# Kernel tuning notes

Measured on AMD Instinct MI355X. Metric: run time of the kernel, lower is better.

The kernel has to match this reference:

```python
import jax, jax.numpy as jnp
import numpy as np

N_NODES = 50000
NEG_SLOPE = 0.2

def _segment_softmax(e, seg, n):
    m = jax.ops.segment_max(e, seg, num_segments=n)
    ex = jnp.exp(e - m[seg])
    s = jax.ops.segment_sum(ex, seg, num_segments=n)
    return ex / s[seg]

def _gatv2_layer(x, src, dst, n, Wl, bl, Wr, br, att):
    # GATv2 (heads=1): e_ij = att . leaky_relu(Wl x_j + Wr x_i); msg = alpha * Wl x_j
    xl = x @ Wl + bl            # [N, D] source transform
    xr = x @ Wr + br            # [N, D] target transform
    h = jax.nn.leaky_relu(xl[src] + xr[dst], NEG_SLOPE)  # [E, D]
    e = h @ att                 # [E]
    alpha = _segment_softmax(e, dst, n)
    out = jax.ops.segment_sum(alpha[:, None] * xl[src], dst, num_segments=n)
    return out

def setup_inputs() -> dict:
    key = jax.random.key(0)
    ks = jax.random.split(key, 16)
    N, E, Q, F, D, H = N_NODES, 800000, 200000, 128, 250, 256
    def glorot(k, shape):
        fan = shape[0] + shape[-1]
        return jax.random.uniform(k, shape, jnp.float32, -1.0, 1.0) * np.sqrt(6.0 / fan)
    return {
        "x": jax.random.normal(ks[0], (N, F), jnp.float32),
        "edge_index": jax.random.randint(ks[1], (2, E), 0, N, jnp.int32),
        "query": jax.random.randint(ks[2], (Q, 2), 0, N, jnp.int32),
        "W1l": glorot(ks[3], (F, D)), "b1l": jnp.zeros((D,), jnp.float32),
        "W1r": glorot(ks[4], (F, D)), "b1r": jnp.zeros((D,), jnp.float32),
        "att1": glorot(ks[5], (D,)),
        "W2l": glorot(ks[6], (D, D)), "b2l": jnp.zeros((D,), jnp.float32),
        "W2r": glorot(ks[7], (D, D)), "b2r": jnp.zeros((D,), jnp.float32),
        "att2": glorot(ks[8], (D,)),
        "Wm1": glorot(ks[9], (2 * D, H)), "bm1": jnp.zeros((H,), jnp.float32),
        "Wm2": glorot(ks[10], (H, 1)), "bm2": jnp.zeros((1,), jnp.float32),
    }

def reference(x, edge_index, query, W1l, b1l, W1r, b1r, att1,
              W2l, b2l, W2r, b2r, att2, Wm1, bm1, Wm2, bm2):
    n = x.shape[0]
    # add self loops (PyG default add_self_loops=True)
    loops = jnp.arange(n, dtype=edge_index.dtype)
    src = jnp.concatenate([edge_index[0], loops])
    dst = jnp.concatenate([edge_index[1], loops])
    h = _gatv2_layer(x, src, dst, n, W1l, b1l, W1r, b1r, att1)
    h = jax.nn.relu(h)
    emb = _gatv2_layer(h, src, dst, n, W2l, b2l, W2r, b2r, att2)
    # edge-prediction head: gather pair embeddings, concat, MLP
    pair = jnp.concatenate([emb[query[:, 0]], emb[query[:, 1]]], axis=1)  # [Q, 2D]
    out = jax.nn.relu(pair @ Wm1 + bm1)
    out = jax.nn.relu(out @ Wm2 + bm2)
    return out
```

## Files before the change

### kernel.cpp

```cpp
#include <hip/hip_runtime.h>
#include <hip/hip_fp16.h>
#include <math.h>
#include <stdint.h>

#define NN 50000
#define NE 800000
#define ET (NE + NN)
#define FIN 128
#define DD 250
#define HD 256
#define NQ 200000
#define NEG_SLOPE 0.2f
#define NPW 4

typedef unsigned short u16;
typedef __attribute__((ext_vector_type(4))) float f32x4;
typedef _Float16 h2v __attribute__((ext_vector_type(2)));
typedef _Float16 f16x8 __attribute__((ext_vector_type(8)));

union H2U { h2v h; unsigned int u; };

__device__ __forceinline__ u16 f2h(float v) {
    __half h = __float2half(v);
    return *reinterpret_cast<u16*>(&h);
}
__device__ __forceinline__ float4 ld4h(const u16* p) {
    uint2 r = *(const uint2*)p;
    __half2 a = *(__half2*)&r.x;
    __half2 b = *(__half2*)&r.y;
    float2 fa = __half22float2(a), fb = __half22float2(b);
    return make_float4(fa.x, fa.y, fb.x, fb.y);
}
__device__ __forceinline__ h2v hmax2v(h2v a, h2v b) {
    return __builtin_elementwise_max(a, b);
}


#define DPPMOV(v, ctrl, rm) \
    ((unsigned int)__builtin_amdgcn_update_dpp(0, (int)(v), (ctrl), (rm), 0xF, true))

__device__ __forceinline__ unsigned int h2_wave_sum63(h2v x) {
    H2U u, t; u.h = x;
    t.u = DPPMOV(u.u, 0x111, 0xF); u.h = u.h + t.h;
    t.u = DPPMOV(u.u, 0x112, 0xF); u.h = u.h + t.h;
    t.u = DPPMOV(u.u, 0x114, 0xF); u.h = u.h + t.h;
    t.u = DPPMOV(u.u, 0x118, 0xF); u.h = u.h + t.h;
    t.u = DPPMOV(u.u, 0x142, 0xA); u.h = u.h + t.h;
    t.u = DPPMOV(u.u, 0x143, 0xC); u.h = u.h + t.h;
    return (unsigned int)__builtin_amdgcn_readlane((int)u.u, 63);
}

__device__ __forceinline__ float f32_wave_sum63(float x) {
    union FU { float f; unsigned int u; } a, t, o;
    a.f = x;
    t.u = DPPMOV(a.u, 0x111, 0xF); a.f += t.f;
    t.u = DPPMOV(a.u, 0x112, 0xF); a.f += t.f;
    t.u = DPPMOV(a.u, 0x114, 0xF); a.f += t.f;
    t.u = DPPMOV(a.u, 0x118, 0xF); a.f += t.f;
    t.u = DPPMOV(a.u, 0x142, 0xA); a.f += t.f;
    t.u = DPPMOV(a.u, 0x143, 0xC); a.f += t.f;
    o.u = (unsigned int)__builtin_amdgcn_readlane((int)a.u, 63);
    return o.f;
}


__global__ __launch_bounds__(256) void scan1_kernel(
    int* __restrict__ cnt, int* __restrict__ rowptr, int* __restrict__ bsum)
{
    __shared__ int buf[256];
    int t = threadIdx.x;
    int i = blockIdx.x * 256 + t;
    int v = (i < NN) ? cnt[i] : 0;
    if (i < NN) cnt[i] = 0;
    buf[t] = v;
    __syncthreads();
#pragma unroll
    for (int off = 1; off < 256; off <<= 1) {
        int add = (t >= off) ? buf[t - off] : 0;
        __syncthreads();
        buf[t] += add;
        __syncthreads();
    }
    if (i < NN) rowptr[i] = buf[t] - v;
    if (t == 255) bsum[blockIdx.x] = buf[255];
}

__global__ __launch_bounds__(256) void scan2_kernel(
    int* __restrict__ bsum, int* __restrict__ rowptr, int nb)
{
    __shared__ int buf[256];
    int t = threadIdx.x;
    int v = (t < nb) ? bsum[t] : 0;
    buf[t] = v;
    __syncthreads();
#pragma unroll
    for (int off = 1; off < 256; off <<= 1) {
        int add = (t >= off) ? buf[t - off] : 0;
        __syncthreads();
        buf[t] += add;
        __syncthreads();
    }
    if (t < nb) bsum[t] = buf[t] - v;
    if (t == 255) rowptr[NN] = buf[255];
}

__global__ __launch_bounds__(256) void scan3_kernel(
    int* __restrict__ rowptr, const int* __restrict__ bsum)
{
    int i = blockIdx.x * 256 + threadIdx.x;
    if (i < NN) rowptr[i] += bsum[blockIdx.x];
}

__global__ void scatter_kernel(const int* __restrict__ ei,
                               const int* __restrict__ rowptr,
                               int* __restrict__ fill,
                               int* __restrict__ ssrc) {
    int k = blockIdx.x * 256 + threadIdx.x;
    if (k >= ET) return;
    int s, d;
    if (k < NE) { s = ei[k]; d = ei[NE + k]; }
    else        { s = k - NE; d = k - NE; }
    int pos = rowptr[d] + atomicAdd(&fill[d], 1);
    ssrc[pos] = s << 9;
}


#define CONVX_BLOCKS 3125
#define CNT_BLOCKS ((ET + 255) / 256)

__global__ __launch_bounds__(256) void conv_all(
    const float* __restrict__ x, const int* __restrict__ ei,
    u16* __restrict__ Asp,
    const float* __restrict__ W1l, const float* __restrict__ W1r,
    const float* __restrict__ W2l, const float* __restrict__ W2r,
    const float* __restrict__ Wm1,
    const float* __restrict__ att1, const float* __restrict__ att2,
    u16* __restrict__ W1lT, u16* __restrict__ W1rT,
    u16* __restrict__ W2lT, u16* __restrict__ W2rT,
    u16* __restrict__ WmtT, u16* __restrict__ WmbT,
    u16* __restrict__ atth1, u16* __restrict__ atth2,
    int* __restrict__ cnt)
{
    if (blockIdx.x < CONVX_BLOCKS) {
        int tid = blockIdx.x * 256 + threadIdx.x;
        size_t idx = (size_t)tid * 8;
        if (idx >= (size_t)NN * FIN) return;
        float4 v0 = *(const float4*)(x + idx);
        float4 v1 = *(const float4*)(x + idx + 4);
        ushort4 o0, o1;
        o0.x = f2h(v0.x); o0.y = f2h(v0.y); o0.z = f2h(v0.z); o0.w = f2h(v0.w);
        o1.x = f2h(v1.x); o1.y = f2h(v1.y); o1.z = f2h(v1.z); o1.w = f2h(v1.w);
        *(ushort4*)(Asp + idx) = o0;
        *(ushort4*)(Asp + idx + 4) = o1;
        return;
    }
    int b = blockIdx.x - CONVX_BLOCKS;
    if (b < 1280) {
        const float* W; int K, N, koff, kshift, b0; u16* ot;
        if (b < 128)       { W = W1l; K = FIN; N = DD; koff = 0;  kshift = 7; b0 = 0;    ot = W1lT; }
        else if (b < 256)  { W = W1r; K = FIN; N = DD; koff = 0;  kshift = 7; b0 = 128;  ot = W1rT; }
        else if (b < 512)  { W = W2l; K = DD;  N = DD; koff = 0;  kshift = 8; b0 = 256;  ot = W2lT; }
        else if (b < 768)  { W = W2r; K = DD;  N = DD; koff = 0;  kshift = 8; b0 = 512;  ot = W2rT; }
        else if (b < 1024) { W = Wm1; K = DD;  N = HD; koff = 0;  kshift = 8; b0 = 768;  ot = WmtT; }
        else               { W = Wm1; K = DD;  N = HD; koff = DD; kshift = 8; b0 = 1024; ot = WmbT; }
        int id = (b - b0) * 256 + threadIdx.x;
        int Kp = 1 << kshift;
        int n = id >> kshift, k = id & (Kp - 1);
        float v = (n < N && k < K) ? W[(size_t)(k + koff) * N + n] : 0.f;
        ot[id] = f2h(v);
        return;
    }
    if (b < 1282) {
        const float* a = (b == 1280) ? att1 : att2;
        u16* o = (b == 1280) ? atth1 : atth2;
        int id = threadIdx.x;
        o[id] = f2h(id < DD ? a[id] : 0.f);
        return;
    }
    int k = (b - 1282) * 256 + threadIdx.x;
    if (k >= ET) return;
    int d = (k < NE) ? ei[NE + k] : (k - NE);
    atomicAdd(&cnt[d], 1);
}


#define AP 40

__global__ __launch_bounds__(512) void gemm_pair(
    const u16* __restrict__ A, int Kp,
    const u16* __restrict__ B0, const u16* __restrict__ B1,
    const float* __restrict__ bias0, const float* __restrict__ bias1,
    void* __restrict__ C0v, void* __restrict__ C1v, int M, int N, int fmt)
{
    __shared__ u16 AS[128][AP], B0S[256][AP], B1S[256][AP];

    int row0 = blockIdx.x * 128;
    int t = threadIdx.x;
    int lane = t & 63, w = t >> 6;
    int wr = w >> 2, wc = w & 3;
    int quad = lane >> 4, rr = lane & 15;

    f32x4 acc0[4][4], acc1[4][4];
#pragma unroll
    for (int i = 0; i < 4; i++)
#pragma unroll
        for (int j = 0; j < 4; j++) {
            acc0[i][j] = (f32x4){0.f, 0.f, 0.f, 0.f};
            acc1[i][j] = (f32x4){0.f, 0.f, 0.f, 0.f};
        }

    int arow = t >> 2, akc = (t & 3) * 8;
    bool aok = (row0 + arow) < M;
    const u16* pA   = A  + (size_t)(row0 + arow) * Kp + akc;
    int brow = t >> 2, bkc = akc;
    const u16* pB0a = B0 + (size_t)brow * Kp + bkc;
    const u16* pB0b = pB0a + (size_t)128 * Kp;
    const u16* pB1a = B1 + (size_t)brow * Kp + bkc;
    const u16* pB1b = pB1a + (size_t)128 * Kp;

    for (int k0 = 0; k0 < Kp; k0 += 32) {
        f16x8 a{};
        if (aok) a = *(const f16x8*)(pA + k0);
        *(f16x8*)&AS[arow][akc]            = a;
        *(f16x8*)&B0S[brow][bkc]           = *(const f16x8*)(pB0a + k0);
        *(f16x8*)&B0S[brow + 128][bkc]     = *(const f16x8*)(pB0b + k0);
        *(f16x8*)&B1S[brow][bkc]           = *(const f16x8*)(pB1a + k0);
        *(f16x8*)&B1S[brow + 128][bkc]     = *(const f16x8*)(pB1b + k0);
        __syncthreads();

        f16x8 fA[4];
#pragma unroll
        for (int fi = 0; fi < 4; fi++) {
            int r = wr * 64 + fi * 16 + rr;
            fA[fi] = *(const f16x8*)&AS[r][quad * 8];
        }
#pragma unroll
        for (int fj = 0; fj < 4; fj++) {
            int c = wc * 64 + fj * 16 + rr;
            f16x8 b0 = *(const f16x8*)&B0S[c][quad * 8];
            f16x8 b1 = *(const f16x8*)&B1S[c][quad * 8];
#pragma unroll
            for (int fi = 0; fi < 4; fi++) {
                acc0[fi][fj] = __builtin_amdgcn_mfma_f32_16x16x32_f16(fA[fi], b0, acc0[fi][fj], 0, 0, 0);
                acc1[fi][fj] = __builtin_amdgcn_mfma_f32_16x16x32_f16(fA[fi], b1, acc1[fi][fj], 0, 0, 0);
            }
        }
        __syncthreads();
    }

#pragma unroll
    for (int fj = 0; fj < 4; fj++) {
        int gc = wc * 64 + fj * 16 + rr;
        if (gc >= N) continue;
        float bb0 = bias0 ? bias0[gc] : 0.f;
        float bb1 = bias1 ? bias1[gc] : 0.f;
#pragma unroll
        for (int fi = 0; fi < 4; fi++) {
#pragma unroll
            for (int r = 0; r < 4; r++) {
                int grr = row0 + wr * 64 + fi * 16 + quad * 4 + r;
                if (grr < M) {
                    float v0 = acc0[fi][fj][r] + bb0;
                    float v1 = acc1[fi][fj][r] + bb1;
                    if (fmt & 1) ((u16*)C0v)[(size_t)grr * 256 + gc] = f2h(v0);
                    else         ((float*)C0v)[(size_t)grr * N + gc] = v0;
                    if (fmt & 2) ((u16*)C1v)[(size_t)grr * 256 + gc] = f2h(v1);
                    else         ((float*)C1v)[(size_t)grr * N + gc] = v1;
                }
            }
        }
    }
}


__global__ __launch_bounds__(256) void fused_edge_kernel(
    const int* __restrict__ rowptr, const int* __restrict__ ssrc,
    const u16* __restrict__ xl16, const u16* __restrict__ xr16,
    const u16* __restrict__ atth,
    u16* __restrict__ Oh, int dorelu)
{
    int wid = blockIdx.x * 4 + (threadIdx.x >> 6);
    int base = wid * NPW;
    if (base >= NN) return;
    int lane = threadIdx.x & 63;
    int d0 = lane * 4;
    int lb = d0 * 2;

    uint2 atr = *(const uint2*)&atth[d0];
    h2v at0h = *(h2v*)&atr.x, at1h = *(h2v*)&atr.y;
    const h2v c02 = {(_Float16)0.2f, (_Float16)0.2f};
    const char* xlb = (const char*)xl16;

    auto ldrow = [&](int o) -> uint2 {
        return *(const uint2*)(xlb + o + lb);
    };

    uint2 xrr = *(const uint2*)&xr16[(size_t)base * 256 + d0];

    for (int k = 0; k < NPW; k++) {
        int i = base + k;
        if (i >= NN) break;
        h2v xr0h = *(h2v*)&xrr.x, xr1h = *(h2v*)&xrr.y;
        int beg = __builtin_amdgcn_readfirstlane(rowptr[i]);
        int end = __builtin_amdgcn_readfirstlane(rowptr[i + 1]);

        float m = -1e30f, ssum = 0.f;
        float4 acc = make_float4(0.f, 0.f, 0.f, 0.f);

        auto edge_score = [&](uint2 g) -> float {
            h2v x0 = *(h2v*)&g.x, x1 = *(h2v*)&g.y;
            h2v s = x0 + xr0h; s = hmax2v(s, s * c02);
            float e = __builtin_amdgcn_fdot2(s, at0h, 0.f, false);
            s = x1 + xr1h; s = hmax2v(s, s * c02);
            return __builtin_amdgcn_fdot2(s, at1h, e, false);
        };
        auto single_update = [&](uint2 g) {
            float e = f32_wave_sum63(edge_score(g));
            h2v x0 = *(h2v*)&g.x, x1 = *(h2v*)&g.y;
            float nm = fmaxf(m, e);
            float sc = __expf(m - nm);
            float w = __expf(e - nm);
            acc.x = fmaf(w, (float)x0.x, acc.x * sc);
            acc.y = fmaf(w, (float)x0.y, acc.y * sc);
            acc.z = fmaf(w, (float)x1.x, acc.z * sc);
            acc.w = fmaf(w, (float)x1.y, acc.w * sc);
            ssum = fmaf(ssum, sc, w);
            m = nm;
        };

        int p = beg;
        if (p + 3 < end) {
            int o0 = __builtin_amdgcn_readfirstlane(ssrc[p]);
            int o1 = __builtin_amdgcn_readfirstlane(ssrc[p + 1]);
            int o2 = __builtin_amdgcn_readfirstlane(ssrc[p + 2]);
            int o3 = __builtin_amdgcn_readfirstlane(ssrc[p + 3]);
            uint2 c0 = ldrow(o0), c1 = ldrow(o1), c2 = ldrow(o2), c3 = ldrow(o3);
            bool hn = (p + 7 < end);
            int no0 = 0, no1 = 0, no2 = 0, no3 = 0;
            if (hn) {
                no0 = __builtin_amdgcn_readfirstlane(ssrc[p + 4]);
                no1 = __builtin_amdgcn_readfirstlane(ssrc[p + 5]);
                no2 = __builtin_amdgcn_readfirstlane(ssrc[p + 6]);
                no3 = __builtin_amdgcn_readfirstlane(ssrc[p + 7]);
            }
            for (;;) {
                uint2 n0, n1, n2, n3;
                if (hn) {
                    n0 = ldrow(no0); n1 = ldrow(no1); n2 = ldrow(no2); n3 = ldrow(no3);
                }
                bool hnn = (p + 11 < end);
                int nn0 = 0, nn1 = 0, nn2 = 0, nn3 = 0;
                if (hnn) {
                    nn0 = __builtin_amdgcn_readfirstlane(ssrc[p + 8]);
                    nn1 = __builtin_amdgcn_readfirstlane(ssrc[p + 9]);
                    nn2 = __builtin_amdgcn_readfirstlane(ssrc[p + 10]);
                    nn3 = __builtin_amdgcn_readfirstlane(ssrc[p + 11]);
                }

                h2v x00 = *(h2v*)&c0.x, x01 = *(h2v*)&c0.y;
                h2v x10 = *(h2v*)&c1.x, x11 = *(h2v*)&c1.y;
                h2v x20 = *(h2v*)&c2.x, x21 = *(h2v*)&c2.y;
                h2v x30 = *(h2v*)&c3.x, x31 = *(h2v*)&c3.y;

                h2v s;
                float e0, e1, e2, e3;
                s = x00 + xr0h; s = hmax2v(s, s * c02);
                e0 = __builtin_amdgcn_fdot2(s, at0h, 0.f, false);
                s = x01 + xr1h; s = hmax2v(s, s * c02);
                e0 = __builtin_amdgcn_fdot2(s, at1h, e0, false);
                s = x10 + xr0h; s = hmax2v(s, s * c02);
                e1 = __builtin_amdgcn_fdot2(s, at0h, 0.f, false);
                s = x11 + xr1h; s = hmax2v(s, s * c02);
                e1 = __builtin_amdgcn_fdot2(s, at1h, e1, false);
                s = x20 + xr0h; s = hmax2v(s, s * c02);
                e2 = __builtin_amdgcn_fdot2(s, at0h, 0.f, false);
                s = x21 + xr1h; s = hmax2v(s, s * c02);
                e2 = __builtin_amdgcn_fdot2(s, at1h, e2, false);
                s = x30 + xr0h; s = hmax2v(s, s * c02);
                e3 = __builtin_amdgcn_fdot2(s, at0h, 0.f, false);
                s = x31 + xr1h; s = hmax2v(s, s * c02);
                e3 = __builtin_amdgcn_fdot2(s, at1h, e3, false);

                H2U u01, u23, r01, r23;
                u01.h.x = (_Float16)e0; u01.h.y = (_Float16)e1;
                u23.h.x = (_Float16)e2; u23.h.y = (_Float16)e3;
                r01.u = h2_wave_sum63(u01.h);
                r23.u = h2_wave_sum63(u23.h);
                float es0 = (float)r01.h.x, es1 = (float)r01.h.y;
                float es2 = (float)r23.h.x, es3 = (float)r23.h.y;

                float nm = fmaxf(fmaxf(m, es0), fmaxf(fmaxf(es1, es2), es3));
                float sc = __expf(m - nm);
                float w0 = __expf(es0 - nm);
                float w1 = __expf(es1 - nm);
                float w2 = __expf(es2 - nm);
                float w3 = __expf(es3 - nm);
                float ax0 = fmaf(w1, (float)x10.x, w0 * (float)x00.x);
                float ax1 = fmaf(w3, (float)x30.x, w2 * (float)x20.x);
                float ay0 = fmaf(w1, (float)x10.y, w0 * (float)x00.y);
                float ay1 = fmaf(w3, (float)x30.y, w2 * (float)x20.y);
                float az0 = fmaf(w1, (float)x11.x, w0 * (float)x01.x);
                float az1 = fmaf(w3, (float)x31.x, w2 * (float)x21.x);
                float aw0 = fmaf(w1, (float)x11.y, w0 * (float)x01.y);
                float aw1 = fmaf(w3, (float)x31.y, w2 * (float)x21.y);
                acc.x = fmaf(acc.x, sc, ax0 + ax1);
                acc.y = fmaf(acc.y, sc, ay0 + ay1);
                acc.z = fmaf(acc.z, sc, az0 + az1);
                acc.w = fmaf(acc.w, sc, aw0 + aw1);
                ssum = fmaf(ssum, sc, (w0 + w1) + (w2 + w3));
                m = nm;

                p += 4;
                if (!hn) break;
                c0 = n0; c1 = n1; c2 = n2; c3 = n3;
                no0 = nn0; no1 = nn1; no2 = nn2; no3 = nn3;
                hn = hnn;
            }
        }

        if (k + 1 < NPW && i + 1 < NN)
            xrr = *(const uint2*)&xr16[(size_t)(i + 1) * 256 + d0];

        int rem = end - p;
        if (rem > 0) {
            int o0 = __builtin_amdgcn_readfirstlane(ssrc[p]);
            int o1 = 0, o2 = 0;
            if (rem > 1) o1 = __builtin_amdgcn_readfirstlane(ssrc[p + 1]);
            if (rem > 2) o2 = __builtin_amdgcn_readfirstlane(ssrc[p + 2]);
            uint2 g0 = ldrow(o0);
            uint2 g1, g2;
            if (rem > 1) g1 = ldrow(o1);
            if (rem > 2) g2 = ldrow(o2);
            single_update(g0);
            if (rem > 1) single_update(g1);
            if (rem > 2) single_update(g2);
        }

        float inv = 1.f / ssum;
        acc.x *= inv; acc.y *= inv; acc.z *= inv; acc.w *= inv;
        if (dorelu) {
            acc.x = fmaxf(acc.x, 0.f); acc.y = fmaxf(acc.y, 0.f);
            acc.z = fmaxf(acc.z, 0.f); acc.w = fmaxf(acc.w, 0.f);
        }
        size_t obase = (size_t)i * 256 + d0;
        ushort4 hv;
        hv.x = f2h(acc.x); hv.y = f2h(acc.y); hv.z = f2h(acc.z); hv.w = f2h(acc.w);
        *(ushort4*)&Oh[obase] = hv;
    }
}


__global__ __launch_bounds__(256) void query_kernel(
    const int* __restrict__ qry, const u16* __restrict__ Ptop,
    const u16* __restrict__ Pbot, const float* __restrict__ Wm2,
    const float* __restrict__ bm2, float* __restrict__ out)
{
    int q = (blockIdx.x * 4 + (threadIdx.x >> 6)) * 2;
    if (q >= NQ) return;
    int lane = threadIdx.x & 63;
    int a0 = __builtin_amdgcn_readfirstlane(qry[q * 2 + 0]);
    int b0 = __builtin_amdgcn_readfirstlane(qry[q * 2 + 1]);
    int a1 = __builtin_amdgcn_readfirstlane(qry[q * 2 + 2]);
    int b1 = __builtin_amdgcn_readfirstlane(qry[q * 2 + 3]);
    float4 w  = *(const float4*)&Wm2[lane * 4];
    float4 t0 = ld4h(&Ptop[(size_t)a0 * HD + lane * 4]);
    float4 v0 = ld4h(&Pbot[(size_t)b0 * HD + lane * 4]);
    float4 t1 = ld4h(&Ptop[(size_t)a1 * HD + lane * 4]);
    float4 v1 = ld4h(&Pbot[(size_t)b1 * HD + lane * 4]);
    float s0 = fmaxf(t0.x + v0.x, 0.f) * w.x + fmaxf(t0.y + v0.y, 0.f) * w.y
             + fmaxf(t0.z + v0.z, 0.f) * w.z + fmaxf(t0.w + v0.w, 0.f) * w.w;
    float s1 = fmaxf(t1.x + v1.x, 0.f) * w.x + fmaxf(t1.y + v1.y, 0.f) * w.y
             + fmaxf(t1.z + v1.z, 0.f) * w.z + fmaxf(t1.w + v1.w, 0.f) * w.w;
    s0 = f32_wave_sum63(s0);
    s1 = f32_wave_sum63(s1);
    if (lane == 0) {
        float bb = bm2[0];
        out[q] = fmaxf(s0 + bb, 0.f);
        if (q + 1 < NQ) out[q + 1] = fmaxf(s1 + bb, 0.f);
    }
}


extern "C" void kernel_launch(void* const* d_in, const int* in_sizes, int n_in,
                              void* d_out, int out_size, void* d_ws, size_t ws_size,
                              hipStream_t stream) {
    const float* x    = (const float*)d_in[0];
    const int*   ei   = (const int*)d_in[1];
    const int*   qry  = (const int*)d_in[2];
    const float* W1l  = (const float*)d_in[3];
    const float* b1l  = (const float*)d_in[4];
    const float* W1r  = (const float*)d_in[5];
    const float* b1r  = (const float*)d_in[6];
    const float* att1 = (const float*)d_in[7];
    const float* W2l  = (const float*)d_in[8];
    const float* b2l  = (const float*)d_in[9];
    const float* W2r  = (const float*)d_in[10];
    const float* b2r  = (const float*)d_in[11];
    const float* att2 = (const float*)d_in[12];
    const float* Wm1  = (const float*)d_in[13];
    const float* bm1  = (const float*)d_in[14];
    const float* Wm2  = (const float*)d_in[15];
    const float* bm2  = (const float*)d_in[16];
    float* out = (float*)d_out;

    u16* xl16    = (u16*)d_ws;
    u16* xr16    = xl16 + (size_t)NN * 256;
    int* rowptr  = (int*)(xr16 + (size_t)NN * 256);
    int* fill    = rowptr + NN + 1;
    int* ssrc    = fill + NN;
    int* bsum    = ssrc + ET;
    u16* atth1   = (u16*)(bsum + 256);
    u16* atth2   = atth1 + 256;
    uintptr_t wp = (uintptr_t)(atth2 + 256);
    wp = (wp + 63) & ~(uintptr_t)63;
    u16* W1lT = (u16*)wp;
    u16* W1rT = W1lT + 256 * 128;
    u16* W2lT = W1rT + 256 * 128;
    u16* W2rT = W2lT + 65536;
    u16* WmtT = W2rT + 65536;
    u16* WmbT = WmtT + 65536;
    u16* Asp  = WmbT + 65536;
    u16* Ptop16 = xl16;
    u16* Pbot16 = xr16;

    dim3 blk(256);
    int gET = (ET + 255) / 256;
    int gNode = (NN + 4 * NPW - 1) / (4 * NPW);
    int nb = (NN + 255) / 256;
    int gg = (NN + 127) / 128;

    hipMemsetAsync(fill, 0, (size_t)NN * sizeof(int), stream);
    conv_all<<<CONVX_BLOCKS + 1282 + gET, blk, 0, stream>>>(x, ei, Asp,
        W1l, W1r, W2l, W2r, Wm1, att1, att2,
        W1lT, W1rT, W2lT, W2rT, WmtT, WmbT, atth1, atth2, fill);

    scan1_kernel<<<nb, blk, 0, stream>>>(fill, rowptr, bsum);
    scan2_kernel<<<1, blk, 0, stream>>>(bsum, rowptr, nb);
    scan3_kernel<<<nb, blk, 0, stream>>>(rowptr, bsum);
    scatter_kernel<<<gET, blk, 0, stream>>>(ei, rowptr, fill, ssrc);

    gemm_pair<<<gg, dim3(512), 0, stream>>>(Asp, 128, W1lT, W1rT,
                                      b1l, b1r, (void*)xl16, (void*)xr16, NN, DD, 3);
    fused_edge_kernel<<<gNode, blk, 0, stream>>>(rowptr, ssrc, xl16, xr16, atth1, Asp, 1);

    gemm_pair<<<gg, dim3(512), 0, stream>>>(Asp, 256, W2lT, W2rT,
                                      b2l, b2r, (void*)xl16, (void*)xr16, NN, DD, 3);
    fused_edge_kernel<<<gNode, blk, 0, stream>>>(rowptr, ssrc, xl16, xr16, atth2, Asp, 0);

    gemm_pair<<<gg, dim3(512), 0, stream>>>(Asp, 256, WmtT, WmbT,
                                      bm1, (const float*)nullptr, (void*)Ptop16, (void*)Pbot16, NN, HD, 3);

    query_kernel<<<(NQ / 2 + 3) / 4, blk, 0, stream>>>(qry, Ptop16, Pbot16, Wm2, bm2, out);
}
```

Measured before the change: 530.6 us.

## Split each node's edges across two waves and merge, single-kernel scan

New measurement: 633.5 us. 19.4% more time.

```diff
diff --git a/kernel.cpp b/kernel.cpp
--- a/kernel.cpp
+++ b/kernel.cpp
@@ -11,7 +11,6 @@
 #define HD 256
 #define NQ 200000
 #define NEG_SLOPE 0.2f
-#define NPW 4
 
 typedef unsigned short u16;
 typedef __attribute__((ext_vector_type(4))) float f32x4;
@@ -64,51 +63,32 @@
 }
 
 
-__global__ __launch_bounds__(256) void scan1_kernel(
-    int* __restrict__ cnt, int* __restrict__ rowptr, int* __restrict__ bsum)
+__global__ __launch_bounds__(1024) void scan_all(
+    int* __restrict__ cnt, int* __restrict__ rowptr)
 {
-    __shared__ int buf[256];
+    __shared__ int buf[1024];
     int t = threadIdx.x;
-    int i = blockIdx.x * 256 + t;
-    int v = (i < NN) ? cnt[i] : 0;
-    if (i < NN) cnt[i] = 0;
-    buf[t] = v;
+    const int CH = (NN + 1023) / 1024;
+    int lo = t * CH, hi = lo + CH;
+    if (hi > NN) hi = NN;
+    int s = 0;
+    for (int j = lo; j < hi; j++) s += cnt[j];
+    buf[t] = s;
     __syncthreads();
-#pragma unroll
-    for (int off = 1; off < 256; off <<= 1) {
+    for (int off = 1; off < 1024; off <<= 1) {
         int add = (t >= off) ? buf[t - off] : 0;
         __syncthreads();
         buf[t] += add;
         __syncthreads();
     }
-    if (i < NN) rowptr[i] = buf[t] - v;
-    if (t == 255) bsum[blockIdx.x] = buf[255];
-}
-
-__global__ __launch_bounds__(256) void scan2_kernel(
-    int* __restrict__ bsum, int* __restrict__ rowptr, int nb)
-{
-    __shared__ int buf[256];
-    int t = threadIdx.x;
-    int v = (t < nb) ? bsum[t] : 0;
-    buf[t] = v;
-    __syncthreads();
-#pragma unroll
-    for (int off = 1; off < 256; off <<= 1) {
-        int add = (t >= off) ? buf[t - off] : 0;
-        __syncthreads();
-        buf[t] += add;
-        __syncthreads();
-    }
-    if (t < nb) bsum[t] = buf[t] - v;
-    if (t == 255) rowptr[NN] = buf[255];
-}
-
-__global__ __launch_bounds__(256) void scan3_kernel(
-    int* __restrict__ rowptr, const int* __restrict__ bsum)
-{
-    int i = blockIdx.x * 256 + threadIdx.x;
-    if (i < NN) rowptr[i] += bsum[blockIdx.x];
+    int run = buf[t] - s;
+    for (int j = lo; j < hi; j++) {
+        int c = cnt[j];
+        rowptr[j] = run;
+        run += c;
+        cnt[j] = 0;
+    }
+    if (t == 1023) rowptr[NN] = buf[1023];
 }
 
 __global__ void scatter_kernel(const int* __restrict__ ei,
@@ -279,10 +259,14 @@
     const u16* __restrict__ atth,
     u16* __restrict__ Oh, int dorelu)
 {
-    int wid = blockIdx.x * 4 + (threadIdx.x >> 6);
-    int base = wid * NPW;
-    if (base >= NN) return;
-    int lane = threadIdx.x & 63;
+    __shared__ float accS[2][2][4][64];
+    __shared__ float msS[2][2][2];
+
+    int t = threadIdx.x;
+    int np = t >> 7;
+    int h  = (t >> 6) & 1;
+    int lane = t & 63;
+    int i = blockIdx.x * 2 + np;
     int d0 = lane * 4;
     int lb = d0 * 2;
 
@@ -291,152 +275,170 @@
     const h2v c02 = {(_Float16)0.2f, (_Float16)0.2f};
     const char* xlb = (const char*)xl16;
 
+    uint2 xrr = *(const uint2*)&xr16[(size_t)i * 256 + d0];
+    h2v xr0h = *(h2v*)&xrr.x, xr1h = *(h2v*)&xrr.y;
+
+    int beg = __builtin_amdgcn_readfirstlane(rowptr[i]);
+    int end = __builtin_amdgcn_readfirstlane(rowptr[i + 1]);
+    int halfn = (end - beg + 1) >> 1;
+    int mb = beg + h * halfn;
+    int me = h ? end : (beg + halfn);
+
+    float m = -1e30f, ssum = 0.f;
+    float4 acc = make_float4(0.f, 0.f, 0.f, 0.f);
+
     auto ldrow = [&](int o) -> uint2 {
         return *(const uint2*)(xlb + o + lb);
     };
-
-    uint2 xrr = *(const uint2*)&xr16[(size_t)base * 256 + d0];
-
-    for (int k = 0; k < NPW; k++) {
-        int i = base + k;
-        if (i >= NN) break;
-        h2v xr0h = *(h2v*)&xrr.x, xr1h = *(h2v*)&xrr.y;
-        int beg = __builtin_amdgcn_readfirstlane(rowptr[i]);
-        int end = __builtin_amdgcn_readfirstlane(rowptr[i + 1]);
-
-        float m = -1e30f, ssum = 0.f;
-        float4 acc = make_float4(0.f, 0.f, 0.f, 0.f);
-
-        auto edge_score = [&](uint2 g) -> float {
-            h2v x0 = *(h2v*)&g.x, x1 = *(h2v*)&g.y;
-            h2v s = x0 + xr0h; s = hmax2v(s, s * c02);
-            float e = __builtin_amdgcn_fdot2(s, at0h, 0.f, false);
-            s = x1 + xr1h; s = hmax2v(s, s * c02);
-            return __builtin_amdgcn_fdot2(s, at1h, e, false);
-        };
-        auto single_update = [&](uint2 g) {
-            float e = f32_wave_sum63(edge_score(g));
-            h2v x0 = *(h2v*)&g.x, x1 = *(h2v*)&g.y;
-            float nm = fmaxf(m, e);
+    auto edge_score = [&](uint2 g) -> float {
+        h2v x0 = *(h2v*)&g.x, x1 = *(h2v*)&g.y;
+        h2v s = x0 + xr0h; s = hmax2v(s, s * c02);
+        float e = __builtin_amdgcn_fdot2(s, at0h, 0.f, false);
+        s = x1 + xr1h; s = hmax2v(s, s * c02);
+        return __builtin_amdgcn_fdot2(s, at1h, e, false);
+    };
+    auto single_update = [&](uint2 g) {
+        float e = f32_wave_sum63(edge_score(g));
+        h2v x0 = *(h2v*)&g.x, x1 = *(h2v*)&g.y;
+        float nm = fmaxf(m, e);
+        float sc = __expf(m - nm);
+        float w = __expf(e - nm);
+        acc.x = fmaf(w, (float)x0.x, acc.x * sc);
+        acc.y = fmaf(w, (float)x0.y, acc.y * sc);
+        acc.z = fmaf(w, (float)x1.x, acc.z * sc);
+        acc.w = fmaf(w, (float)x1.y, acc.w * sc);
+        ssum = fmaf(ssum, sc, w);
+        m = nm;
+    };
+
+    int p = mb;
+    if (p + 3 < me) {
+        int o0 = __builtin_amdgcn_readfirstlane(ssrc[p]);
+        int o1 = __builtin_amdgcn_readfirstlane(ssrc[p + 1]);
+        int o2 = __builtin_amdgcn_readfirstlane(ssrc[p + 2]);
+        int o3 = __builtin_amdgcn_readfirstlane(ssrc[p + 3]);
+        uint2 c0 = ldrow(o0), c1 = ldrow(o1), c2 = ldrow(o2), c3 = ldrow(o3);
+        bool hn = (p + 7 < me);
+        int no0 = 0, no1 = 0, no2 = 0, no3 = 0;
+        if (hn) {
+            no0 = __builtin_amdgcn_readfirstlane(ssrc[p + 4]);
+            no1 = __builtin_amdgcn_readfirstlane(ssrc[p + 5]);
+            no2 = __builtin_amdgcn_readfirstlane(ssrc[p + 6]);
+            no3 = __builtin_amdgcn_readfirstlane(ssrc[p + 7]);
+        }
+        for (;;) {
+            uint2 n0, n1, n2, n3;
+            if (hn) {
+                n0 = ldrow(no0); n1 = ldrow(no1); n2 = ldrow(no2); n3 = ldrow(no3);
+            }
+            bool hnn = (p + 11 < me);
+            int nn0 = 0, nn1 = 0, nn2 = 0, nn3 = 0;
+            if (hnn) {
+                nn0 = __builtin_amdgcn_readfirstlane(ssrc[p + 8]);
+                nn1 = __builtin_amdgcn_readfirstlane(ssrc[p + 9]);
+                nn2 = __builtin_amdgcn_readfirstlane(ssrc[p + 10]);
+                nn3 = __builtin_amdgcn_readfirstlane(ssrc[p + 11]);
+            }
+
+            h2v x00 = *(h2v*)&c0.x, x01 = *(h2v*)&c0.y;
+            h2v x10 = *(h2v*)&c1.x, x11 = *(h2v*)&c1.y;
+            h2v x20 = *(h2v*)&c2.x, x21 = *(h2v*)&c2.y;
+            h2v x30 = *(h2v*)&c3.x, x31 = *(h2v*)&c3.y;
+
+            h2v s;
+            float e0, e1, e2, e3;
+            s = x00 + xr0h; s = hmax2v(s, s * c02);
+            e0 = __builtin_amdgcn_fdot2(s, at0h, 0.f, false);
+            s = x01 + xr1h; s = hmax2v(s, s * c02);
+            e0 = __builtin_amdgcn_fdot2(s, at1h, e0, false);
+            s = x10 + xr0h; s = hmax2v(s, s * c02);
+            e1 = __builtin_amdgcn_fdot2(s, at0h, 0.f, false);
+            s = x11 + xr1h; s = hmax2v(s, s * c02);
+            e1 = __builtin_amdgcn_fdot2(s, at1h, e1, false);
+            s = x20 + xr0h; s = hmax2v(s, s * c02);
+            e2 = __builtin_amdgcn_fdot2(s, at0h, 0.f, false);
+            s = x21 + xr1h; s = hmax2v(s, s * c02);
+            e2 = __builtin_amdgcn_fdot2(s, at1h, e2, false);
+            s = x30 + xr0h; s = hmax2v(s, s * c02);
+            e3 = __builtin_amdgcn_fdot2(s, at0h, 0.f, false);
+            s = x31 + xr1h; s = hmax2v(s, s * c02);
+            e3 = __builtin_amdgcn_fdot2(s, at1h, e3, false);
+
+            H2U u01, u23, r01, r23;
+            u01.h.x = (_Float16)e0; u01.h.y = (_Float16)e1;
+            u23.h.x = (_Float16)e2; u23.h.y = (_Float16)e3;
+            r01.u = h2_wave_sum63(u01.h);
+            r23.u = h2_wave_sum63(u23.h);
+            float es0 = (float)r01.h.x, es1 = (float)r01.h.y;
+            float es2 = (float)r23.h.x, es3 = (float)r23.h.y;
+
+            float nm = fmaxf(fmaxf(m, es0), fmaxf(fmaxf(es1, es2), es3));
             float sc = __expf(m - nm);
-            float w = __expf(e - nm);
-            acc.x = fmaf(w, (float)x0.x, acc.x * sc);
-            acc.y = fmaf(w, (float)x0.y, acc.y * sc);
-            acc.z = fmaf(w, (float)x1.x, acc.z * sc);
-            acc.w = fmaf(w, (float)x1.y, acc.w * sc);
-            ssum = fmaf(ssum, sc, w);
+            float w0 = __expf(es0 - nm);
+            float w1 = __expf(es1 - nm);
+            float w2 = __expf(es2 - nm);
+            float w3 = __expf(es3 - nm);
+            float ax0 = fmaf(w1, (float)x10.x, w0 * (float)x00.x);
+            float ax1 = fmaf(w3, (float)x30.x, w2 * (float)x20.x);
+            float ay0 = fmaf(w1, (float)x10.y, w0 * (float)x00.y);
+            float ay1 = fmaf(w3, (float)x30.y, w2 * (float)x20.y);
+            float az0 = fmaf(w1, (float)x11.x, w0 * (float)x01.x);
+            float az1 = fmaf(w3, (float)x31.x, w2 * (float)x21.x);
+            float aw0 = fmaf(w1, (float)x11.y, w0 * (float)x01.y);
+            float aw1 = fmaf(w3, (float)x31.y, w2 * (float)x21.y);
+            acc.x = fmaf(acc.x, sc, ax0 + ax1);
+            acc.y = fmaf(acc.y, sc, ay0 + ay1);
+            acc.z = fmaf(acc.z, sc, az0 + az1);
+            acc.w = fmaf(acc.w, sc, aw0 + aw1);
+            ssum = fmaf(ssum, sc, (w0 + w1) + (w2 + w3));
             m = nm;
-        };
-
-        int p = beg;
-        if (p + 3 < end) {
-            int o0 = __builtin_amdgcn_readfirstlane(ssrc[p]);
-            int o1 = __builtin_amdgcn_readfirstlane(ssrc[p + 1]);
-            int o2 = __builtin_amdgcn_readfirstlane(ssrc[p + 2]);
-            int o3 = __builtin_amdgcn_readfirstlane(ssrc[p + 3]);
-            uint2 c0 = ldrow(o0), c1 = ldrow(o1), c2 = ldrow(o2), c3 = ldrow(o3);
-            bool hn = (p + 7 < end);
-            int no0 = 0, no1 = 0, no2 = 0, no3 = 0;
-            if (hn) {
-                no0 = __builtin_amdgcn_readfirstlane(ssrc[p + 4]);
-                no1 = __builtin_amdgcn_readfirstlane(ssrc[p + 5]);
-                no2 = __builtin_amdgcn_readfirstlane(ssrc[p + 6]);
-                no3 = __builtin_amdgcn_readfirstlane(ssrc[p + 7]);
-            }
-            for (;;) {
-                uint2 n0, n1, n2, n3;
-                if (hn) {
-                    n0 = ldrow(no0); n1 = ldrow(no1); n2 = ldrow(no2); n3 = ldrow(no3);
-                }
-                bool hnn = (p + 11 < end);
-                int nn0 = 0, nn1 = 0, nn2 = 0, nn3 = 0;
-                if (hnn) {
-                    nn0 = __builtin_amdgcn_readfirstlane(ssrc[p + 8]);
-                    nn1 = __builtin_amdgcn_readfirstlane(ssrc[p + 9]);
-                    nn2 = __builtin_amdgcn_readfirstlane(ssrc[p + 10]);
-                    nn3 = __builtin_amdgcn_readfirstlane(ssrc[p + 11]);
-                }
-
-                h2v x00 = *(h2v*)&c0.x, x01 = *(h2v*)&c0.y;
-                h2v x10 = *(h2v*)&c1.x, x11 = *(h2v*)&c1.y;
-                h2v x20 = *(h2v*)&c2.x, x21 = *(h2v*)&c2.y;
-                h2v x30 = *(h2v*)&c3.x, x31 = *(h2v*)&c3.y;
-
-                h2v s;
-                float e0, e1, e2, e3;
-                s = x00 + xr0h; s = hmax2v(s, s * c02);
-                e0 = __builtin_amdgcn_fdot2(s, at0h, 0.f, false);
-                s = x01 + xr1h; s = hmax2v(s, s * c02);
-                e0 = __builtin_amdgcn_fdot2(s, at1h, e0, false);
-                s = x10 + xr0h; s = hmax2v(s, s * c02);
-                e1 = __builtin_amdgcn_fdot2(s, at0h, 0.f, false);
-                s = x11 + xr1h; s = hmax2v(s, s * c02);
-                e1 = __builtin_amdgcn_fdot2(s, at1h, e1, false);
-                s = x20 + xr0h; s = hmax2v(s, s * c02);
-                e2 = __builtin_amdgcn_fdot2(s, at0h, 0.f, false);
-                s = x21 + xr1h; s = hmax2v(s, s * c02);
-                e2 = __builtin_amdgcn_fdot2(s, at1h, e2, false);
-                s = x30 + xr0h; s = hmax2v(s, s * c02);
-                e3 = __builtin_amdgcn_fdot2(s, at0h, 0.f, false);
-                s = x31 + xr1h; s = hmax2v(s, s * c02);
-                e3 = __builtin_amdgcn_fdot2(s, at1h, e3, false);
-
-                H2U u01, u23, r01, r23;
-                u01.h.x = (_Float16)e0; u01.h.y = (_Float16)e1;
-                u23.h.x = (_Float16)e2; u23.h.y = (_Float16)e3;
-                r01.u = h2_wave_sum63(u01.h);
-                r23.u = h2_wave_sum63(u23.h);
-                float es0 = (float)r01.h.x, es1 = (float)r01.h.y;
-                float es2 = (float)r23.h.x, es3 = (float)r23.h.y;
-
-                float nm = fmaxf(fmaxf(m, es0), fmaxf(fmaxf(es1, es2), es3));
-                float sc = __expf(m - nm);
-                float w0 = __expf(es0 - nm);
-                float w1 = __expf(es1 - nm);
-                float w2 = __expf(es2 - nm);
-                float w3 = __expf(es3 - nm);
-                float ax0 = fmaf(w1, (float)x10.x, w0 * (float)x00.x);
-                float ax1 = fmaf(w3, (float)x30.x, w2 * (float)x20.x);
-                float ay0 = fmaf(w1, (float)x10.y, w0 * (float)x00.y);
-                float ay1 = fmaf(w3, (float)x30.y, w2 * (float)x20.y);
-                float az0 = fmaf(w1, (float)x11.x, w0 * (float)x01.x);
-                float az1 = fmaf(w3, (float)x31.x, w2 * (float)x21.x);
-                float aw0 = fmaf(w1, (float)x11.y, w0 * (float)x01.y);
-                float aw1 = fmaf(w3, (float)x31.y, w2 * (float)x21.y);
-                acc.x = fmaf(acc.x, sc, ax0 + ax1);
-                acc.y = fmaf(acc.y, sc, ay0 + ay1);
-                acc.z = fmaf(acc.z, sc, az0 + az1);
-                acc.w = fmaf(acc.w, sc, aw0 + aw1);
-                ssum = fmaf(ssum, sc, (w0 + w1) + (w2 + w3));
-                m = nm;
-
-                p += 4;
-                if (!hn) break;
-                c0 = n0; c1 = n1; c2 = n2; c3 = n3;
-                no0 = nn0; no1 = nn1; no2 = nn2; no3 = nn3;
-                hn = hnn;
-            }
-        }
-
-        if (k + 1 < NPW && i + 1 < NN)
-            xrr = *(const uint2*)&xr16[(size_t)(i + 1) * 256 + d0];
-
-        int rem = end - p;
-        if (rem > 0) {
-            int o0 = __builtin_amdgcn_readfirstlane(ssrc[p]);
-            int o1 = 0, o2 = 0;
-            if (rem > 1) o1 = __builtin_amdgcn_readfirstlane(ssrc[p + 1]);
-            if (rem > 2) o2 = __builtin_amdgcn_readfirstlane(ssrc[p + 2]);
-            uint2 g0 = ldrow(o0);
-            uint2 g1, g2;
-            if (rem > 1) g1 = ldrow(o1);
-            if (rem > 2) g2 = ldrow(o2);
-            single_update(g0);
-            if (rem > 1) single_update(g1);
-            if (rem > 2) single_update(g2);
-        }
-
-        float inv = 1.f / ssum;
+
+            p += 4;
+            if (!hn) break;
+            c0 = n0; c1 = n1; c2 = n2; c3 = n3;
+            no0 = nn0; no1 = nn1; no2 = nn2; no3 = nn3;
+            hn = hnn;
+        }
+    }
+
+    int rem = me - p;
+    if (rem > 0) {
+        int o0 = __builtin_amdgcn_readfirstlane(ssrc[p]);
+        int o1 = 0, o2 = 0;
+        if (rem > 1) o1 = __builtin_amdgcn_readfirstlane(ssrc[p + 1]);
+        if (rem > 2) o2 = __builtin_amdgcn_readfirstlane(ssrc[p + 2]);
+        uint2 g0 = ldrow(o0);
+        uint2 g1, g2;
+        if (rem > 1) g1 = ldrow(o1);
+        if (rem > 2) g2 = ldrow(o2);
+        single_update(g0);
+        if (rem > 1) single_update(g1);
+        if (rem > 2) single_update(g2);
+    }
+
+    accS[np][h][0][lane] = acc.x;
+    accS[np][h][1][lane] = acc.y;
+    accS[np][h][2][lane] = acc.z;
+    accS[np][h][3][lane] = acc.w;
+    if (lane == 0) { msS[np][h][0] = m; msS[np][h][1] = ssum; }
+    __syncthreads();
+    if (h == 0) {
+        float m2 = msS[np][1][0], s2 = msS[np][1][1];
+        float M = fmaxf(m, m2);
+        float w1 = __expf(m - M);
+        float w2 = __expf(m2 - M);
+        float S = ssum * w1 + s2 * w2;
+        float4 a2;
+        a2.x = accS[np][1][0][lane];
+        a2.y = accS[np][1][1][lane];
+        a2.z = accS[np][1][2][lane];
+        a2.w = accS[np][1][3][lane];
+        acc.x = acc.x * w1 + a2.x * w2;
+        acc.y = acc.y * w1 + a2.y * w2;
+        acc.z = acc.z * w1 + a2.z * w2;
+        acc.w = acc.w * w1 + a2.w * w2;
+
+        float inv = 1.f / S;
         acc.x *= inv; acc.y *= inv; acc.z *= inv; acc.w *= inv;
         if (dorelu) {
             acc.x = fmaxf(acc.x, 0.f); acc.y = fmaxf(acc.y, 0.f);
@@ -525,8 +527,7 @@
 
     dim3 blk(256);
     int gET = (ET + 255) / 256;
-    int gNode = (NN + 4 * NPW - 1) / (4 * NPW);
-    int nb = (NN + 255) / 256;
+    int gNode = NN / 2;
     int gg = (NN + 127) / 128;
 
     hipMemsetAsync(fill, 0, (size_t)NN * sizeof(int), stream);
@@ -534,9 +535,7 @@
         W1l, W1r, W2l, W2r, Wm1, att1, att2,
         W1lT, W1rT, W2lT, W2rT, WmtT, WmbT, atth1, atth2, fill);
 
-    scan1_kernel<<<nb, blk, 0, stream>>>(fill, rowptr, bsum);
-    scan2_kernel<<<1, blk, 0, stream>>>(bsum, rowptr, nb);
-    scan3_kernel<<<nb, blk, 0, stream>>>(rowptr, bsum);
+    scan_all<<<1, dim3(1024), 0, stream>>>(fill, rowptr);
     scatter_kernel<<<gET, blk, 0, stream>>>(ei, rowptr, fill, ssrc);
 
     gemm_pair<<<gg, dim3(512), 0, stream>>>(Asp, 128, W1lT, W1rT,
```

## Use one node per wave and deepen edge-row prefetch to two groups

Applied to the files above, without the earlier changes.

Measured after the change: 511.8 us. 1.04x faster.

```diff
diff --git a/kernel.cpp b/kernel.cpp
--- a/kernel.cpp
+++ b/kernel.cpp
@@ -11,7 +11,6 @@
 #define HD 256
 #define NQ 200000
 #define NEG_SLOPE 0.2f
-#define NPW 4
 
 typedef unsigned short u16;
 typedef __attribute__((ext_vector_type(4))) float f32x4;
@@ -126,7 +125,6 @@
 
 
 #define CONVX_BLOCKS 3125
-#define CNT_BLOCKS ((ET + 255) / 256)
 
 __global__ __launch_bounds__(256) void conv_all(
     const float* __restrict__ x, const int* __restrict__ ei,
@@ -279,9 +277,8 @@
     const u16* __restrict__ atth,
     u16* __restrict__ Oh, int dorelu)
 {
-    int wid = blockIdx.x * 4 + (threadIdx.x >> 6);
-    int base = wid * NPW;
-    if (base >= NN) return;
+    int i = blockIdx.x * 4 + (threadIdx.x >> 6);
+    if (i >= NN) return;
     int lane = threadIdx.x & 63;
     int d0 = lane * 4;
     int lb = d0 * 2;
@@ -291,162 +288,166 @@
     const h2v c02 = {(_Float16)0.2f, (_Float16)0.2f};
     const char* xlb = (const char*)xl16;
 
+    uint2 xrr = *(const uint2*)&xr16[(size_t)i * 256 + d0];
+    h2v xr0h = *(h2v*)&xrr.x, xr1h = *(h2v*)&xrr.y;
+
+    int beg = __builtin_amdgcn_readfirstlane(rowptr[i]);
+    int end = __builtin_amdgcn_readfirstlane(rowptr[i + 1]);
+
+    float m = -1e30f, ssum = 0.f;
+    float4 acc = make_float4(0.f, 0.f, 0.f, 0.f);
+
     auto ldrow = [&](int o) -> uint2 {
         return *(const uint2*)(xlb + o + lb);
     };
-
-    uint2 xrr = *(const uint2*)&xr16[(size_t)base * 256 + d0];
-
-    for (int k = 0; k < NPW; k++) {
-        int i = base + k;
-        if (i >= NN) break;
-        h2v xr0h = *(h2v*)&xrr.x, xr1h = *(h2v*)&xrr.y;
-        int beg = __builtin_amdgcn_readfirstlane(rowptr[i]);
-        int end = __builtin_amdgcn_readfirstlane(rowptr[i + 1]);
-
-        float m = -1e30f, ssum = 0.f;
-        float4 acc = make_float4(0.f, 0.f, 0.f, 0.f);
-
-        auto edge_score = [&](uint2 g) -> float {
-            h2v x0 = *(h2v*)&g.x, x1 = *(h2v*)&g.y;
-            h2v s = x0 + xr0h; s = hmax2v(s, s * c02);
-            float e = __builtin_amdgcn_fdot2(s, at0h, 0.f, false);
-            s = x1 + xr1h; s = hmax2v(s, s * c02);
-            return __builtin_amdgcn_fdot2(s, at1h, e, false);
-        };
-        auto single_update = [&](uint2 g) {
-            float e = f32_wave_sum63(edge_score(g));
-            h2v x0 = *(h2v*)&g.x, x1 = *(h2v*)&g.y;
-            float nm = fmaxf(m, e);
+    auto edge_score = [&](uint2 g) -> float {
+        h2v x0 = *(h2v*)&g.x, x1 = *(h2v*)&g.y;
+        h2v s = x0 + xr0h; s = hmax2v(s, s * c02);
+        float e = __builtin_amdgcn_fdot2(s, at0h, 0.f, false);
+        s = x1 + xr1h; s = hmax2v(s, s * c02);
+        return __builtin_amdgcn_fdot2(s, at1h, e, false);
+    };
+    auto single_update = [&](uint2 g) {
+        float e = f32_wave_sum63(edge_score(g));
+        h2v x0 = *(h2v*)&g.x, x1 = *(h2v*)&g.y;
+        float nm = fmaxf(m, e);
+        float sc = __expf(m - nm);
+        float w = __expf(e - nm);
+        acc.x = fmaf(w, (float)x0.x, acc.x * sc);
+        acc.y = fmaf(w, (float)x0.y, acc.y * sc);
+        acc.z = fmaf(w, (float)x1.x, acc.z * sc);
+        acc.w = fmaf(w, (float)x1.y, acc.w * sc);
+        ssum = fmaf(ssum, sc, w);
+        m = nm;
+    };
+
+    int p = beg;
+    if (p + 3 < end) {
+        int o0 = __builtin_amdgcn_readfirstlane(ssrc[p]);
+        int o1 = __builtin_amdgcn_readfirstlane(ssrc[p + 1]);
+        int o2 = __builtin_amdgcn_readfirstlane(ssrc[p + 2]);
+        int o3 = __builtin_amdgcn_readfirstlane(ssrc[p + 3]);
+        uint2 a0 = ldrow(o0), a1 = ldrow(o1), a2 = ldrow(o2), a3 = ldrow(o3);
+
+        bool hB = (p + 7 < end);
+        uint2 b0, b1, b2, b3;
+        if (hB) {
+            int q0 = __builtin_amdgcn_readfirstlane(ssrc[p + 4]);
+            int q1 = __builtin_amdgcn_readfirstlane(ssrc[p + 5]);
+            int q2 = __builtin_amdgcn_readfirstlane(ssrc[p + 6]);
+            int q3 = __builtin_amdgcn_readfirstlane(ssrc[p + 7]);
+            b0 = ldrow(q0); b1 = ldrow(q1); b2 = ldrow(q2); b3 = ldrow(q3);
+        }
+        bool hC = (p + 11 < end);
+        int co0 = 0, co1 = 0, co2 = 0, co3 = 0;
+        if (hC) {
+            co0 = __builtin_amdgcn_readfirstlane(ssrc[p + 8]);
+            co1 = __builtin_amdgcn_readfirstlane(ssrc[p + 9]);
+            co2 = __builtin_amdgcn_readfirstlane(ssrc[p + 10]);
+            co3 = __builtin_amdgcn_readfirstlane(ssrc[p + 11]);
+        }
+
+        for (;;) {
+            uint2 cg0, cg1, cg2, cg3;
+            if (hC) {
+                cg0 = ldrow(co0); cg1 = ldrow(co1); cg2 = ldrow(co2); cg3 = ldrow(co3);
+            }
+            bool hD = (p + 15 < end);
+            int do0 = 0, do1 = 0, do2 = 0, do3 = 0;
+            if (hD) {
+                do0 = __builtin_amdgcn_readfirstlane(ssrc[p + 12]);
+                do1 = __builtin_amdgcn_readfirstlane(ssrc[p + 13]);
+                do2 = __builtin_amdgcn_readfirstlane(ssrc[p + 14]);
+                do3 = __builtin_amdgcn_readfirstlane(ssrc[p + 15]);
+            }
+
+            h2v x00 = *(h2v*)&a0.x, x01 = *(h2v*)&a0.y;
+            h2v x10 = *(h2v*)&a1.x, x11 = *(h2v*)&a1.y;
+            h2v x20 = *(h2v*)&a2.x, x21 = *(h2v*)&a2.y;
+            h2v x30 = *(h2v*)&a3.x, x31 = *(h2v*)&a3.y;
+
+            h2v s;
+            float e0, e1, e2, e3;
+            s = x00 + xr0h; s = hmax2v(s, s * c02);
+            e0 = __builtin_amdgcn_fdot2(s, at0h, 0.f, false);
+            s = x01 + xr1h; s = hmax2v(s, s * c02);
+            e0 = __builtin_amdgcn_fdot2(s, at1h, e0, false);
+            s = x10 + xr0h; s = hmax2v(s, s * c02);
+            e1 = __builtin_amdgcn_fdot2(s, at0h, 0.f, false);
+            s = x11 + xr1h; s = hmax2v(s, s * c02);
+            e1 = __builtin_amdgcn_fdot2(s, at1h, e1, false);
+            s = x20 + xr0h; s = hmax2v(s, s * c02);
+            e2 = __builtin_amdgcn_fdot2(s, at0h, 0.f, false);
+            s = x21 + xr1h; s = hmax2v(s, s * c02);
+            e2 = __builtin_amdgcn_fdot2(s, at1h, e2, false);
+            s = x30 + xr0h; s = hmax2v(s, s * c02);
+            e3 = __builtin_amdgcn_fdot2(s, at0h, 0.f, false);
+            s = x31 + xr1h; s = hmax2v(s, s * c02);
+            e3 = __builtin_amdgcn_fdot2(s, at1h, e3, false);
+
+            H2U u01, u23, r01, r23;
+            u01.h.x = (_Float16)e0; u01.h.y = (_Float16)e1;
+            u23.h.x = (_Float16)e2; u23.h.y = (_Float16)e3;
+            r01.u = h2_wave_sum63(u01.h);
+            r23.u = h2_wave_sum63(u23.h);
+            float es0 = (float)r01.h.x, es1 = (float)r01.h.y;
+            float es2 = (float)r23.h.x, es3 = (float)r23.h.y;
+
+            float nm = fmaxf(fmaxf(m, es0), fmaxf(fmaxf(es1, es2), es3));
             float sc = __expf(m - nm);
-            float w = __expf(e - nm);
-            acc.x = fmaf(w, (float)x0.x, acc.x * sc);
-            acc.y = fmaf(w, (float)x0.y, acc.y * sc);
-            acc.z = fmaf(w, (float)x1.x, acc.z * sc);
-            acc.w = fmaf(w, (float)x1.y, acc.w * sc);
-            ssum = fmaf(ssum, sc, w);
+            float w0 = __expf(es0 - nm);
+            float w1 = __expf(es1 - nm);
+            float w2 = __expf(es2 - nm);
+            float w3 = __expf(es3 - nm);
+            float ax0 = fmaf(w1, (float)x10.x, w0 * (float)x00.x);
+            float ax1 = fmaf(w3, (float)x30.x, w2 * (float)x20.x);
+            float ay0 = fmaf(w1, (float)x10.y, w0 * (float)x00.y);
+            float ay1 = fmaf(w3, (float)x30.y, w2 * (float)x20.y);
+            float az0 = fmaf(w1, (float)x11.x, w0 * (float)x01.x);
+            float az1 = fmaf(w3, (float)x31.x, w2 * (float)x21.x);
+            float aw0 = fmaf(w1, (float)x11.y, w0 * (float)x01.y);
+            float aw1 = fmaf(w3, (float)x31.y, w2 * (float)x21.y);
+            acc.x = fmaf(acc.x, sc, ax0 + ax1);
+            acc.y = fmaf(acc.y, sc, ay0 + ay1);
+            acc.z = fmaf(acc.z, sc, az0 + az1);
+            acc.w = fmaf(acc.w, sc, aw0 + aw1);
+            ssum = fmaf(ssum, sc, (w0 + w1) + (w2 + w3));
             m = nm;
-        };
-
-        int p = beg;
-        if (p + 3 < end) {
-            int o0 = __builtin_amdgcn_readfirstlane(ssrc[p]);
-            int o1 = __builtin_amdgcn_readfirstlane(ssrc[p + 1]);
-            int o2 = __builtin_amdgcn_readfirstlane(ssrc[p + 2]);
-            int o3 = __builtin_amdgcn_readfirstlane(ssrc[p + 3]);
-            uint2 c0 = ldrow(o0), c1 = ldrow(o1), c2 = ldrow(o2), c3 = ldrow(o3);
-            bool hn = (p + 7 < end);
-            int no0 = 0, no1 = 0, no2 = 0, no3 = 0;
-            if (hn) {
-                no0 = __builtin_amdgcn_readfirstlane(ssrc[p + 4]);
-                no1 = __builtin_amdgcn_readfirstlane(ssrc[p + 5]);
-                no2 = __builtin_amdgcn_readfirstlane(ssrc[p + 6]);
-                no3 = __builtin_amdgcn_readfirstlane(ssrc[p + 7]);
-            }
-            for (;;) {
-                uint2 n0, n1, n2, n3;
-                if (hn) {
-                    n0 = ldrow(no0); n1 = ldrow(no1); n2 = ldrow(no2); n3 = ldrow(no3);
-                }
-                bool hnn = (p + 11 < end);
-                int nn0 = 0, nn1 = 0, nn2 = 0, nn3 = 0;
-                if (hnn) {
-                    nn0 = __builtin_amdgcn_readfirstlane(ssrc[p + 8]);
-                    nn1 = __builtin_amdgcn_readfirstlane(ssrc[p + 9]);
-                    nn2 = __builtin_amdgcn_readfirstlane(ssrc[p + 10]);
-                    nn3 = __builtin_amdgcn_readfirstlane(ssrc[p + 11]);
-                }
-
-                h2v x00 = *(h2v*)&c0.x, x01 = *(h2v*)&c0.y;
-                h2v x10 = *(h2v*)&c1.x, x11 = *(h2v*)&c1.y;
-                h2v x20 = *(h2v*)&c2.x, x21 = *(h2v*)&c2.y;
-                h2v x30 = *(h2v*)&c3.x, x31 = *(h2v*)&c3.y;
-
-                h2v s;
-                float e0, e1, e2, e3;
-                s = x00 + xr0h; s = hmax2v(s, s * c02);
-                e0 = __builtin_amdgcn_fdot2(s, at0h, 0.f, false);
-                s = x01 + xr1h; s = hmax2v(s, s * c02);
-                e0 = __builtin_amdgcn_fdot2(s, at1h, e0, false);
-                s = x10 + xr0h; s = hmax2v(s, s * c02);
-                e1 = __builtin_amdgcn_fdot2(s, at0h, 0.f, false);
-                s = x11 + xr1h; s = hmax2v(s, s * c02);
-                e1 = __builtin_amdgcn_fdot2(s, at1h, e1, false);
-                s = x20 + xr0h; s = hmax2v(s, s * c02);
-                e2 = __builtin_amdgcn_fdot2(s, at0h, 0.f, false);
-                s = x21 + xr1h; s = hmax2v(s, s * c02);
-                e2 = __builtin_amdgcn_fdot2(s, at1h, e2, false);
-                s = x30 + xr0h; s = hmax2v(s, s * c02);
-                e3 = __builtin_amdgcn_fdot2(s, at0h, 0.f, false);
-                s = x31 + xr1h; s = hmax2v(s, s * c02);
-                e3 = __builtin_amdgcn_fdot2(s, at1h, e3, false);
-
-                H2U u01, u23, r01, r23;
-                u01.h.x = (_Float16)e0; u01.h.y = (_Float16)e1;
-                u23.h.x = (_Float16)e2; u23.h.y = (_Float16)e3;
-                r01.u = h2_wave_sum63(u01.h);
-                r23.u = h2_wave_sum63(u23.h);
-                float es0 = (float)r01.h.x, es1 = (float)r01.h.y;
-                float es2 = (float)r23.h.x, es3 = (float)r23.h.y;
-
-                float nm = fmaxf(fmaxf(m, es0), fmaxf(fmaxf(es1, es2), es3));
-                float sc = __expf(m - nm);
-                float w0 = __expf(es0 - nm);
-                float w1 = __expf(es1 - nm);
-                float w2 = __expf(es2 - nm);
-                float w3 = __expf(es3 - nm);
-                float ax0 = fmaf(w1, (float)x10.x, w0 * (float)x00.x);
-                float ax1 = fmaf(w3, (float)x30.x, w2 * (float)x20.x);
-                float ay0 = fmaf(w1, (float)x10.y, w0 * (float)x00.y);
-                float ay1 = fmaf(w3, (float)x30.y, w2 * (float)x20.y);
-                float az0 = fmaf(w1, (float)x11.x, w0 * (float)x01.x);
-                float az1 = fmaf(w3, (float)x31.x, w2 * (float)x21.x);
-                float aw0 = fmaf(w1, (float)x11.y, w0 * (float)x01.y);
-                float aw1 = fmaf(w3, (float)x31.y, w2 * (float)x21.y);
-                acc.x = fmaf(acc.x, sc, ax0 + ax1);
-                acc.y = fmaf(acc.y, sc, ay0 + ay1);
-                acc.z = fmaf(acc.z, sc, az0 + az1);
-                acc.w = fmaf(acc.w, sc, aw0 + aw1);
-                ssum = fmaf(ssum, sc, (w0 + w1) + (w2 + w3));
-                m = nm;
-
-                p += 4;
-                if (!hn) break;
-                c0 = n0; c1 = n1; c2 = n2; c3 = n3;
-                no0 = nn0; no1 = nn1; no2 = nn2; no3 = nn3;
-                hn = hnn;
-            }
-        }
-
-        if (k + 1 < NPW && i + 1 < NN)
-            xrr = *(const uint2*)&xr16[(size_t)(i + 1) * 256 + d0];
-
-        int rem = end - p;
-        if (rem > 0) {
-            int o0 = __builtin_amdgcn_readfirstlane(ssrc[p]);
-            int o1 = 0, o2 = 0;
-            if (rem > 1) o1 = __builtin_amdgcn_readfirstlane(ssrc[p + 1]);
-            if (rem > 2) o2 = __builtin_amdgcn_readfirstlane(ssrc[p + 2]);
-            uint2 g0 = ldrow(o0);
-            uint2 g1, g2;
-            if (rem > 1) g1 = ldrow(o1);
-            if (rem > 2) g2 = ldrow(o2);
-            single_update(g0);
-            if (rem > 1) single_update(g1);
-            if (rem > 2) single_update(g2);
-        }
-
-        float inv = 1.f / ssum;
-        acc.x *= inv; acc.y *= inv; acc.z *= inv; acc.w *= inv;
-        if (dorelu) {
-            acc.x = fmaxf(acc.x, 0.f); acc.y = fmaxf(acc.y, 0.f);
-            acc.z = fmaxf(acc.z, 0.f); acc.w = fmaxf(acc.w, 0.f);
-        }
-        size_t obase = (size_t)i * 256 + d0;
-        ushort4 hv;
-        hv.x = f2h(acc.x); hv.y = f2h(acc.y); hv.z = f2h(acc.z); hv.w = f2h(acc.w);
-        *(ushort4*)&Oh[obase] = hv;
-    }
+
+            p += 4;
+            if (!hB) break;
+            a0 = b0; a1 = b1; a2 = b2; a3 = b3;
+            b0 = cg0; b1 = cg1; b2 = cg2; b3 = cg3;
+            hB = hC; hC = hD;
+            co0 = do0; co1 = do1; co2 = do2; co3 = do3;
+        }
+    }
+
+    int rem = end - p;
+    if (rem > 0) {
+        int o0 = __builtin_amdgcn_readfirstlane(ssrc[p]);
+        int o1 = 0, o2 = 0;
+        if (rem > 1) o1 = __builtin_amdgcn_readfirstlane(ssrc[p + 1]);
+        if (rem > 2) o2 = __builtin_amdgcn_readfirstlane(ssrc[p + 2]);
+        uint2 g0 = ldrow(o0);
+        uint2 g1, g2;
+        if (rem > 1) g1 = ldrow(o1);
+        if (rem > 2) g2 = ldrow(o2);
+        single_update(g0);
+        if (rem > 1) single_update(g1);
+        if (rem > 2) single_update(g2);
+    }
+
+    float inv = 1.f / ssum;
+    acc.x *= inv; acc.y *= inv; acc.z *= inv; acc.w *= inv;
+    if (dorelu) {
+        acc.x = fmaxf(acc.x, 0.f); acc.y = fmaxf(acc.y, 0.f);
+        acc.z = fmaxf(acc.z, 0.f); acc.w = fmaxf(acc.w, 0.f);
+    }
+    size_t obase = (size_t)i * 256 + d0;
+    ushort4 hv;
+    hv.x = f2h(acc.x); hv.y = f2h(acc.y); hv.z = f2h(acc.z); hv.w = f2h(acc.w);
+    *(ushort4*)&Oh[obase] = hv;
 }
 
 
@@ -525,7 +526,7 @@
 
     dim3 blk(256);
     int gET = (ET + 255) / 256;
-    int gNode = (NN + 4 * NPW - 1) / (4 * NPW);
+    int gNode = (NN + 3) / 4;
     int nb = (NN + 255) / 256;
     int gg = (NN + 127) / 128;
 
```
